# Kernel optimization log

Measured on AMD Instinct MI355X. Metric: run time of the kernel, lower is better.

The kernel has to match this reference:

```python
import jax, jax.numpy as jnp
import numpy as np

D = 1024
H = 16
HD = D // H  # 64


def setup_inputs() -> dict:
    key = jax.random.key(0)
    ks = jax.random.split(key, 12)
    B, S = 2, 2048
    inp = {
        "input_query": jax.random.normal(ks[0], (B, S, D), jnp.float32),
        "input_key": jax.random.normal(ks[1], (B, S, D), jnp.float32),
        "input_value": jax.random.normal(ks[2], (B, S, D), jnp.float32),
        "mask": jnp.ones((S, S), dtype=bool),  # ignored, as in original
        # per-head Q/K/V linears, stacked over heads: [H, D, HD]
        "Wq": jax.random.normal(ks[3], (H, D, HD), jnp.float32) / np.sqrt(D),
        "bq": jax.random.normal(ks[4], (H, HD), jnp.float32) * 0.01,
        "Wk": jax.random.normal(ks[5], (H, D, HD), jnp.float32) / np.sqrt(D),
        "bk": jax.random.normal(ks[6], (H, HD), jnp.float32) * 0.01,
        "Wv": jax.random.normal(ks[7], (H, D, HD), jnp.float32) / np.sqrt(D),
        "bv": jax.random.normal(ks[8], (H, HD), jnp.float32) * 0.01,
        "Wo": jax.random.normal(ks[9], (D, D), jnp.float32) / np.sqrt(D),
        "bo": jax.random.normal(ks[10], (D,), jnp.float32) * 0.01,
    }
    return inp


def reference(input_query, input_key, input_value, mask, Wq, bq, Wk, bk, Wv, bv, Wo, bo):
    B, S, _ = input_query.shape
    # batched per-head projections: [B,S,D] x [H,D,HD] -> [B,H,S,HD]
    q = jnp.einsum("bsd,hdk->bhsk", input_query, Wq) + bq[None, :, None, :]
    k = jnp.einsum("bsd,hdk->bhsk", input_key, Wk) + bk[None, :, None, :]
    v = jnp.einsum("bsd,hdk->bhsk", input_value, Wv) + bv[None, :, None, :]
    scale = 1.0 / np.sqrt(HD)
    scores = jnp.einsum("bhqk,bhsk->bhqs", q, k) * scale  # [B,H,S,S]
    causal = jnp.tril(jnp.ones((S, S), dtype=bool))
    scores = jnp.where(causal[None, None], scores, jnp.finfo(scores.dtype).min)
    p = jax.nn.softmax(scores, axis=-1)
    out = jnp.einsum("bhqs,bhsk->bhqk", p, v)  # [B,H,S,HD]
    # concat heads (matches torch.cat over head outputs on last dim)
    out = out.transpose(0, 2, 1, 3).reshape(B, S, D)
    return out @ Wo + bo
```

## Files before the change

kernel.cpp:

```cpp
#include <hip/hip_runtime.h>
#include <hip/hip_bf16.h>

typedef __bf16 bf16;
typedef bf16 bf16x8 __attribute__((ext_vector_type(8)));
typedef bf16 bf16x4 __attribute__((ext_vector_type(4)));
typedef float f32x4 __attribute__((ext_vector_type(4)));

#define B_  2
#define S_  2048
#define D_  1024
#define H_  16
#define HD_ 64
#define M_  4096
#define K_  1024
#define N_  1024

#if __has_builtin(__builtin_amdgcn_exp2f)
#define EXP2F(x) __builtin_amdgcn_exp2f(x)
#else
#define EXP2F(x) exp2f(x)
#endif

__device__ __forceinline__ void gld16(const bf16* g, bf16* l) {
    __builtin_amdgcn_global_load_lds(
        (const __attribute__((address_space(1))) unsigned int*)(g),
        (__attribute__((address_space(3))) unsigned int*)(l), 16, 0, 0);
}
__device__ __forceinline__ void gld16f(const float* g, float* l) {
    __builtin_amdgcn_global_load_lds(
        (const __attribute__((address_space(1))) unsigned int*)(g),
        (__attribute__((address_space(3))) unsigned int*)(l), 16, 0, 0);
}

__global__ void pack_w(const float* __restrict__ wq, const float* __restrict__ wk,
                       const float* __restrict__ wv, const float* __restrict__ wo,
                       bf16* __restrict__ out) {
    int t = blockIdx.y;
    bf16* dst = out + (size_t)t * N_ * K_;
    int o = blockIdx.x * 256 + threadIdx.x;
    int n = o >> 10, k = o & 1023;
    if (t == 3) {
        dst[o] = (bf16)wo[k * D_ + n];
    } else {
        const float* src = (t == 0) ? wq : (t == 1) ? wk : wv;
        dst[o] = (bf16)src[(n >> 6) * (D_ * HD_) + k * HD_ + (n & 63)];
    }
}

__global__ __launch_bounds__(256) void gemm_qkv(
        const float* __restrict__ xq, const float* __restrict__ xk,
        const float* __restrict__ xv, const bf16* __restrict__ Wt,
        const float* __restrict__ bq, const float* __restrict__ bk,
        const float* __restrict__ bv, bf16* __restrict__ QKV) {
    __shared__ __align__(16) float Af[2][128 * 32];
    __shared__ __align__(16) bf16 Bs[2][128 * 32];
    int t = blockIdx.z;
    const float* A = (t == 0) ? xq : (t == 1) ? xk : xv;
    const bf16* W = Wt + (size_t)t * N_ * K_;
    const float* bias = (t == 0) ? bq : (t == 1) ? bk : bv;
    int m0 = blockIdx.x * 128, n0 = blockIdx.y * 128;
    int tid = threadIdx.x;
    int w = tid >> 6, l = tid & 63, lr = l & 15, lg = l >> 4;
    int wr = (w >> 1) * 64, wc = (w & 1) * 64;
    int srow = (l >> 2), scol = (l & 3) * 8;
    size_t aoff[4];
    #pragma unroll
    for (int c = 0; c < 4; c++) {
        int chunk = w * 256 + c * 64 + l;
        int r = chunk >> 3, p = chunk & 7;
        aoff[c] = (size_t)(m0 + r) * K_ + ((p ^ (r & 7)) << 2);
    }
    f32x4 acc[4][4] = {};
    #pragma unroll
    for (int c = 0; c < 4; c++)
        gld16f(A + aoff[c], &Af[0][(w * 256 + c * 64) * 4]);
    #pragma unroll
    for (int c = 0; c < 2; c++) {
        int chunk = w * 2 + c;
        gld16(&W[(size_t)(n0 + chunk * 16 + srow) * K_ + scol], &Bs[0][chunk * 512]);
    }
    __syncthreads();
    for (int k0 = 0; k0 < K_; k0 += 32) {
        int cur = (k0 >> 5) & 1, nxt = cur ^ 1;
        if (k0 + 32 < K_) {
            #pragma unroll
            for (int c = 0; c < 4; c++)
                gld16f(A + aoff[c] + k0 + 32, &Af[nxt][(w * 256 + c * 64) * 4]);
            #pragma unroll
            for (int c = 0; c < 2; c++) {
                int chunk = w * 2 + c;
                gld16(&W[(size_t)(n0 + chunk * 16 + srow) * K_ + k0 + 32 + scol], &Bs[nxt][chunk * 512]);
            }
        }
        bf16x8 af[4], bfr[4];
        #pragma unroll
        for (int mi = 0; mi < 4; mi++) {
            int r = wr + mi * 16 + lr;
            f32x4 a0 = *(const f32x4*)((const char*)Af[cur] + r * 128 + (((lg * 2) ^ (r & 7)) * 16));
            f32x4 a1 = *(const f32x4*)((const char*)Af[cur] + r * 128 + (((lg * 2 + 1) ^ (r & 7)) * 16));
            bf16x8 v = { (bf16)a0[0], (bf16)a0[1], (bf16)a0[2], (bf16)a0[3],
                         (bf16)a1[0], (bf16)a1[1], (bf16)a1[2], (bf16)a1[3] };
            af[mi] = v;
        }
        #pragma unroll
        for (int ni = 0; ni < 4; ni++) bfr[ni] = *(const bf16x8*)&Bs[cur][(wc + ni * 16 + lr) * 32 + lg * 8];
        #pragma unroll
        for (int mi = 0; mi < 4; mi++)
            #pragma unroll
            for (int ni = 0; ni < 4; ni++)
                acc[mi][ni] = __builtin_amdgcn_mfma_f32_16x16x32_bf16(af[mi], bfr[ni], acc[mi][ni], 0, 0, 0);
        __syncthreads();
    }
    float qscale = (t == 0) ? 0.125f * 1.4426950408889634f : 1.0f;
    #pragma unroll
    for (int mi = 0; mi < 4; mi++)
        #pragma unroll
        for (int ni = 0; ni < 4; ni++)
            #pragma unroll
            for (int i = 0; i < 4; i++) {
                int m = m0 + wr + mi * 16 + lg * 4 + i;
                int n = n0 + wc + ni * 16 + lr;
                float v = (acc[mi][ni][i] + bias[n]) * qscale;
                int b = m >> 11, s = m & 2047, h = n >> 6, hd = n & 63;
                QKV[((((size_t)t * B_ + b) * H_ + h) * S_ + s) * HD_ + hd] = (bf16)v;
            }
}

__global__ __launch_bounds__(256) void gemm_out(
        const bf16* __restrict__ A, const bf16* __restrict__ Wt,
        const float* __restrict__ bo, float* __restrict__ out) {
    __shared__ __align__(16) bf16 As[2][128 * 32];
    __shared__ __align__(16) bf16 Bs[2][128 * 32];
    int m0 = blockIdx.x * 128, n0 = blockIdx.y * 128;
    int tid = threadIdx.x;
    int w = tid >> 6, l = tid & 63, lr = l & 15, lg = l >> 4;
    int wr = (w >> 1) * 64, wc = (w & 1) * 64;
    int srow = (l >> 2), scol = (l & 3) * 8;
    f32x4 acc[4][4] = {};
    #pragma unroll
    for (int c = 0; c < 2; c++) {
        int chunk = w * 2 + c;
        gld16(&A[(size_t)(m0 + chunk * 16 + srow) * K_ + scol], &As[0][chunk * 512]);
        gld16(&Wt[(size_t)(n0 + chunk * 16 + srow) * K_ + scol], &Bs[0][chunk * 512]);
    }
    __syncthreads();
    for (int k0 = 0; k0 < K_; k0 += 32) {
        int cur = (k0 >> 5) & 1, nxt = cur ^ 1;
        if (k0 + 32 < K_) {
            #pragma unroll
            for (int c = 0; c < 2; c++) {
                int chunk = w * 2 + c;
                gld16(&A[(size_t)(m0 + chunk * 16 + srow) * K_ + k0 + 32 + scol], &As[nxt][chunk * 512]);
                gld16(&Wt[(size_t)(n0 + chunk * 16 + srow) * K_ + k0 + 32 + scol], &Bs[nxt][chunk * 512]);
            }
        }
        bf16x8 af[4], bfr[4];
        #pragma unroll
        for (int mi = 0; mi < 4; mi++) af[mi] = *(const bf16x8*)&As[cur][(wr + mi * 16 + lr) * 32 + lg * 8];
        #pragma unroll
        for (int ni = 0; ni < 4; ni++) bfr[ni] = *(const bf16x8*)&Bs[cur][(wc + ni * 16 + lr) * 32 + lg * 8];
        #pragma unroll
        for (int mi = 0; mi < 4; mi++)
            #pragma unroll
            for (int ni = 0; ni < 4; ni++)
                acc[mi][ni] = __builtin_amdgcn_mfma_f32_16x16x32_bf16(af[mi], bfr[ni], acc[mi][ni], 0, 0, 0);
        __syncthreads();
    }
    #pragma unroll
    for (int mi = 0; mi < 4; mi++)
        #pragma unroll
        for (int ni = 0; ni < 4; ni++)
            #pragma unroll
            for (int i = 0; i < 4; i++) {
                int m = m0 + wr + mi * 16 + lg * 4 + i;
                int n = n0 + wc + ni * 16 + lr;
                out[(size_t)m * N_ + n] = acc[mi][ni][i] + bo[n];
            }
}

__global__ __launch_bounds__(256) void transpose_v(const bf16* __restrict__ V,
                                                   bf16* __restrict__ VT) {
    __shared__ __align__(16) bf16 Ls[64][64];
    int s0 = blockIdx.x * 64, bh = blockIdx.y;
    const bf16* src = V + (size_t)bh * S_ * HD_;
    bf16* dst = VT + (size_t)bh * HD_ * S_;
    int tid = threadIdx.x;
    #pragma unroll
    for (int c = tid; c < 512; c += 256) {
        int row = c >> 3, cg = (c & 7) * 8;
        int cgp = cg ^ (((row >> 3) & 3) << 4);
        *(bf16x8*)&Ls[row][cgp] = *(const bf16x8*)&src[(size_t)(s0 + row) * 64 + cg];
    }
    __syncthreads();
    #pragma unroll
    for (int c = tid; c < 512; c += 256) {
        int hd = c >> 3, sg = (c & 7) * 8;
        bf16x8 v;
        #pragma unroll
        for (int e = 0; e < 8; e++) {
            int row = sg + e;
            v[e] = Ls[row][hd ^ (((row >> 3) & 3) << 4)];
        }
        *(bf16x8*)&dst[(size_t)hd * S_ + s0 + sg] = v;
    }
}

__global__ __launch_bounds__(512) void attn(const bf16* __restrict__ QKV,
                                            const bf16* __restrict__ VT,
                                            bf16* __restrict__ AO) {
    __shared__ __align__(16) bf16 Ks[2][64][72];
    __shared__ __align__(16) bf16 Vts[2][64][72];
    __shared__ __align__(16) bf16 Ps[8][16][72];
    int bh = blockIdx.y;
    int qt = (bh & 16) ? blockIdx.x : (15 - blockIdx.x);
    int q0 = qt * 128;
    const bf16* Qp = QKV + (size_t)bh * S_ * HD_;
    const bf16* Kp = QKV + (size_t)(32 + bh) * S_ * HD_;
    const bf16* VTp = VT + (size_t)bh * HD_ * S_;
    int tid = threadIdx.x, w = tid >> 6, l = tid & 63, lr = l & 15, lg = l >> 4;
    int srow = tid >> 3, scg = (tid & 7) * 8;

    bf16x8 aq[2];
    #pragma unroll
    for (int ks = 0; ks < 2; ks++)
        aq[ks] = *(const bf16x8*)&Qp[(size_t)(q0 + w * 16 + lr) * 64 + ks * 32 + lg * 8];

    f32x4 o[4] = {};
    float lsum[4] = {};
    int jmax = 2 * qt + 1;

    *(bf16x8*)&Ks[0][srow][scg]  = *(const bf16x8*)&Kp[(size_t)srow * 64 + scg];
    *(bf16x8*)&Vts[0][srow][scg] = *(const bf16x8*)&VTp[(size_t)srow * S_ + scg];
    __syncthreads();

    for (int j = 0; j <= jmax; ++j) {
        int cur = j & 1;
        bool pf = (j < jmax);
        bf16x8 kreg, vreg;
        if (pf) {
            kreg = *(const bf16x8*)&Kp[(size_t)((j + 1) * 64 + srow) * 64 + scg];
            vreg = *(const bf16x8*)&VTp[(size_t)srow * S_ + (j + 1) * 64 + scg];
        }

        f32x4 sc[4] = {};
        __builtin_amdgcn_s_setprio(1);
        #pragma unroll
        for (int ks = 0; ks < 2; ks++)
            #pragma unroll
            for (int ni = 0; ni < 4; ni++) {
                bf16x8 bk_ = *(const bf16x8*)&Ks[cur][ni * 16 + lr][ks * 32 + lg * 8];
                sc[ni] = __builtin_amdgcn_mfma_f32_16x16x32_bf16(aq[ks], bk_, sc[ni], 0, 0, 0);
            }
        __builtin_amdgcn_s_setprio(0);

        bool diag = (j >= 2 * qt);
        int qrow = w * 16 + lg * 4;
        int kvb = j * 64 - q0;
        #pragma unroll
        for (int ni = 0; ni < 4; ni++)
            #pragma unroll
            for (int i = 0; i < 4; i++) {
                float s = sc[ni][i];
                if (diag && (kvb + ni * 16 + lr > qrow + i)) s = -30000.0f;
                float p = EXP2F(s);
                lsum[i] += p;
                Ps[w][lg * 4 + i][ni * 16 + lr] = (bf16)p;
            }

        __builtin_amdgcn_s_setprio(1);
        #pragma unroll
        for (int ks = 0; ks < 2; ks++) {
            bf16x8 ap = *(const bf16x8*)&Ps[w][lr][ks * 32 + lg * 8];
            #pragma unroll
            for (int nf = 0; nf < 4; nf++) {
                bf16x8 bv_ = *(const bf16x8*)&Vts[cur][nf * 16 + lr][ks * 32 + lg * 8];
                o[nf] = __builtin_amdgcn_mfma_f32_16x16x32_bf16(ap, bv_, o[nf], 0, 0, 0);
            }
        }
        __builtin_amdgcn_s_setprio(0);

        if (pf) {
            *(bf16x8*)&Ks[cur ^ 1][srow][scg]  = kreg;
            *(bf16x8*)&Vts[cur ^ 1][srow][scg] = vreg;
        }
        __syncthreads();
    }

    #pragma unroll
    for (int i = 0; i < 4; i++) {
        #pragma unroll
        for (int xm = 1; xm < 16; xm <<= 1) lsum[i] += __shfl_xor(lsum[i], xm);
    }

    int b = bh >> 4, h = bh & 15;
    #pragma unroll
    for (int i = 0; i < 4; i++) {
        float inv = 1.0f / lsum[i];
        #pragma unroll
        for (int nf = 0; nf < 4; nf++) {
            int m = b * S_ + q0 + w * 16 + lg * 4 + i;
            int d = h * 64 + nf * 16 + lr;
            AO[(size_t)m * D_ + d] = (bf16)(o[nf][i] * inv);
        }
    }
}

extern "C" void kernel_launch(void* const* d_in, const int* in_sizes, int n_in,
                              void* d_out, int out_size, void* d_ws, size_t ws_size,
                              hipStream_t stream) {
    const float* xq = (const float*)d_in[0];
    const float* xk = (const float*)d_in[1];
    const float* xv = (const float*)d_in[2];
    const float* wq = (const float*)d_in[4];
    const float* bq = (const float*)d_in[5];
    const float* wk = (const float*)d_in[6];
    const float* bk = (const float*)d_in[7];
    const float* wv = (const float*)d_in[8];
    const float* bv = (const float*)d_in[9];
    const float* wo = (const float*)d_in[10];
    const float* bo = (const float*)d_in[11];
    float* out = (float*)d_out;

    bf16* Xb  = (bf16*)d_ws;
    bf16* Wb  = Xb  + (size_t)3 * M_ * K_;
    bf16* WoT = Wb  + (size_t)3 * N_ * K_;
    bf16* QKV = WoT + (size_t)N_ * K_;
    bf16* AO  = QKV + (size_t)3 * M_ * K_;
    bf16* VT  = Xb;

    pack_w <<<dim3(N_ * K_ / 256, 4), 256, 0, stream>>>(wq, wk, wv, wo, Wb);
    gemm_qkv<<<dim3(M_ / 128, N_ / 128, 3), 256, 0, stream>>>(xq, xk, xv, Wb, bq, bk, bv, QKV);
    transpose_v<<<dim3(S_ / 64, B_ * H_), 256, 0, stream>>>(QKV + (size_t)2 * M_ * K_, VT);
    attn    <<<dim3(S_ / 128, B_ * H_), 512, 0, stream>>>(QKV, VT, AO);
    gemm_out<<<dim3(M_ / 128, N_ / 128), 256, 0, stream>>>(AO, WoT, bo, out);
}
```

Baseline: 131.5 us.

## Convert QKV activations to bf16 in registers and swizzle LDS tiles

The QKV projection GEMM now loads fp32 activations into registers, converts them to bf16, and writes them to a padded bf16 LDS tile. Before, the fp32 data was staged in LDS through direct global-to-LDS loads and converted on every fragment read. Both GEMMs also apply an XOR swizzle to the weight (and output A) LDS tiles to reduce bank conflicts, and peel the last k-step out of the loop. This halves LDS footprint for A in the QKV kernel, but the register-staged loads may expose global latency that the async LDS path hid.

```diff
diff --git a/kernel.cpp b/kernel.cpp
--- a/kernel.cpp
+++ b/kernel.cpp
@@ -22,11 +22,6 @@
 #endif
 
 __device__ __forceinline__ void gld16(const bf16* g, bf16* l) {
-    __builtin_amdgcn_global_load_lds(
-        (const __attribute__((address_space(1))) unsigned int*)(g),
-        (__attribute__((address_space(3))) unsigned int*)(l), 16, 0, 0);
-}
-__device__ __forceinline__ void gld16f(const float* g, float* l) {
     __builtin_amdgcn_global_load_lds(
         (const __attribute__((address_space(1))) unsigned int*)(g),
         (__attribute__((address_space(3))) unsigned int*)(l), 16, 0, 0);
@@ -52,7 +47,7 @@
         const float* __restrict__ xv, const bf16* __restrict__ Wt,
         const float* __restrict__ bq, const float* __restrict__ bk,
         const float* __restrict__ bv, bf16* __restrict__ QKV) {
-    __shared__ __align__(16) float Af[2][128 * 32];
+    __shared__ __align__(16) bf16 As[2][128 * 40];
     __shared__ __align__(16) bf16 Bs[2][128 * 32];
     int t = blockIdx.z;
     const float* A = (t == 0) ? xq : (t == 1) ? xk : xv;
@@ -62,55 +57,81 @@
     int tid = threadIdx.x;
     int w = tid >> 6, l = tid & 63, lr = l & 15, lg = l >> 4;
     int wr = (w >> 1) * 64, wc = (w & 1) * 64;
-    int srow = (l >> 2), scol = (l & 3) * 8;
-    size_t aoff[4];
-    #pragma unroll
-    for (int c = 0; c < 4; c++) {
-        int chunk = w * 256 + c * 64 + l;
-        int r = chunk >> 3, p = chunk & 7;
-        aoff[c] = (size_t)(m0 + r) * K_ + ((p ^ (r & 7)) << 2);
-    }
+    int ar = tid >> 1, ah = tid & 1;
+    const float* agp = A + (size_t)(m0 + ar) * K_ + ah * 16;
+    int awb = ar * 80 + ah * 32;
+    int srow = l >> 2;
+    int sscol = ((l & 3) ^ ((srow >> 1) & 3)) * 8;
+    int boff[4];
+    #pragma unroll
+    for (int ni = 0; ni < 4; ni++) {
+        int row = wc + ni * 16 + lr;
+        boff[ni] = row * 64 + ((lg ^ ((row >> 1) & 3)) * 16);
+    }
+    int aoffr[4];
+    #pragma unroll
+    for (int mi = 0; mi < 4; mi++) aoffr[mi] = (wr + mi * 16 + lr) * 80 + lg * 16;
+
     f32x4 acc[4][4] = {};
-    #pragma unroll
-    for (int c = 0; c < 4; c++)
-        gld16f(A + aoff[c], &Af[0][(w * 256 + c * 64) * 4]);
-    #pragma unroll
-    for (int c = 0; c < 2; c++) {
-        int chunk = w * 2 + c;
-        gld16(&W[(size_t)(n0 + chunk * 16 + srow) * K_ + scol], &Bs[0][chunk * 512]);
+
+    {
+        float4 av0 = *(const float4*)(agp + 0);
+        float4 av1 = *(const float4*)(agp + 4);
+        float4 av2 = *(const float4*)(agp + 8);
+        float4 av3 = *(const float4*)(agp + 12);
+        #pragma unroll
+        for (int c = 0; c < 2; c++) {
+            int chunk = w * 2 + c;
+            gld16(&W[(size_t)(n0 + chunk * 16 + srow) * K_ + sscol], &Bs[0][chunk * 512]);
+        }
+        bf16x8 b0 = { (bf16)av0.x, (bf16)av0.y, (bf16)av0.z, (bf16)av0.w,
+                      (bf16)av1.x, (bf16)av1.y, (bf16)av1.z, (bf16)av1.w };
+        bf16x8 b1 = { (bf16)av2.x, (bf16)av2.y, (bf16)av2.z, (bf16)av2.w,
+                      (bf16)av3.x, (bf16)av3.y, (bf16)av3.z, (bf16)av3.w };
+        *(bf16x8*)((char*)As[0] + awb)      = b0;
+        *(bf16x8*)((char*)As[0] + awb + 16) = b1;
     }
     __syncthreads();
-    for (int k0 = 0; k0 < K_; k0 += 32) {
-        int cur = (k0 >> 5) & 1, nxt = cur ^ 1;
-        if (k0 + 32 < K_) {
-            #pragma unroll
-            for (int c = 0; c < 4; c++)
-                gld16f(A + aoff[c] + k0 + 32, &Af[nxt][(w * 256 + c * 64) * 4]);
-            #pragma unroll
-            for (int c = 0; c < 2; c++) {
-                int chunk = w * 2 + c;
-                gld16(&W[(size_t)(n0 + chunk * 16 + srow) * K_ + k0 + 32 + scol], &Bs[nxt][chunk * 512]);
-            }
-        }
+
+    auto do_step = [&](int cb, int k0) {
         bf16x8 af[4], bfr[4];
         #pragma unroll
-        for (int mi = 0; mi < 4; mi++) {
-            int r = wr + mi * 16 + lr;
-            f32x4 a0 = *(const f32x4*)((const char*)Af[cur] + r * 128 + (((lg * 2) ^ (r & 7)) * 16));
-            f32x4 a1 = *(const f32x4*)((const char*)Af[cur] + r * 128 + (((lg * 2 + 1) ^ (r & 7)) * 16));
-            bf16x8 v = { (bf16)a0[0], (bf16)a0[1], (bf16)a0[2], (bf16)a0[3],
-                         (bf16)a1[0], (bf16)a1[1], (bf16)a1[2], (bf16)a1[3] };
-            af[mi] = v;
-        }
-        #pragma unroll
-        for (int ni = 0; ni < 4; ni++) bfr[ni] = *(const bf16x8*)&Bs[cur][(wc + ni * 16 + lr) * 32 + lg * 8];
+        for (int mi = 0; mi < 4; mi++)
+            af[mi] = *(const bf16x8*)((const char*)As[cb] + aoffr[mi]);
+        #pragma unroll
+        for (int ni = 0; ni < 4; ni++)
+            bfr[ni] = *(const bf16x8*)((const char*)Bs[cb] + boff[ni]);
         #pragma unroll
         for (int mi = 0; mi < 4; mi++)
             #pragma unroll
             for (int ni = 0; ni < 4; ni++)
                 acc[mi][ni] = __builtin_amdgcn_mfma_f32_16x16x32_bf16(af[mi], bfr[ni], acc[mi][ni], 0, 0, 0);
+    };
+
+    int cur = 0;
+    for (int k0 = 0; k0 < K_ - 32; k0 += 32) {
+        int nxt = cur ^ 1;
+        float4 av0 = *(const float4*)(agp + k0 + 32);
+        float4 av1 = *(const float4*)(agp + k0 + 36);
+        float4 av2 = *(const float4*)(agp + k0 + 40);
+        float4 av3 = *(const float4*)(agp + k0 + 44);
+        #pragma unroll
+        for (int c = 0; c < 2; c++) {
+            int chunk = w * 2 + c;
+            gld16(&W[(size_t)(n0 + chunk * 16 + srow) * K_ + k0 + 32 + sscol], &Bs[nxt][chunk * 512]);
+        }
+        do_step(cur, k0);
+        bf16x8 b0 = { (bf16)av0.x, (bf16)av0.y, (bf16)av0.z, (bf16)av0.w,
+                      (bf16)av1.x, (bf16)av1.y, (bf16)av1.z, (bf16)av1.w };
+        bf16x8 b1 = { (bf16)av2.x, (bf16)av2.y, (bf16)av2.z, (bf16)av2.w,
+                      (bf16)av3.x, (bf16)av3.y, (bf16)av3.z, (bf16)av3.w };
+        *(bf16x8*)((char*)As[nxt] + awb)      = b0;
+        *(bf16x8*)((char*)As[nxt] + awb + 16) = b1;
         __syncthreads();
-    }
+        cur = nxt;
+    }
+    do_step(cur, K_ - 32);
+
     float qscale = (t == 0) ? 0.125f * 1.4426950408889634f : 1.0f;
     #pragma unroll
     for (int mi = 0; mi < 4; mi++)
@@ -135,37 +156,52 @@
     int tid = threadIdx.x;
     int w = tid >> 6, l = tid & 63, lr = l & 15, lg = l >> 4;
     int wr = (w >> 1) * 64, wc = (w & 1) * 64;
-    int srow = (l >> 2), scol = (l & 3) * 8;
+    int srow = l >> 2;
+    int sscol = ((l & 3) ^ ((srow >> 1) & 3)) * 8;
+    int aoff[4], boff[4];
+    #pragma unroll
+    for (int i = 0; i < 4; i++) {
+        int ra = wr + i * 16 + lr, rb = wc + i * 16 + lr;
+        aoff[i] = ra * 64 + ((lg ^ ((ra >> 1) & 3)) * 16);
+        boff[i] = rb * 64 + ((lg ^ ((rb >> 1) & 3)) * 16);
+    }
     f32x4 acc[4][4] = {};
     #pragma unroll
     for (int c = 0; c < 2; c++) {
         int chunk = w * 2 + c;
-        gld16(&A[(size_t)(m0 + chunk * 16 + srow) * K_ + scol], &As[0][chunk * 512]);
-        gld16(&Wt[(size_t)(n0 + chunk * 16 + srow) * K_ + scol], &Bs[0][chunk * 512]);
+        gld16(&A[(size_t)(m0 + chunk * 16 + srow) * K_ + sscol], &As[0][chunk * 512]);
+        gld16(&Wt[(size_t)(n0 + chunk * 16 + srow) * K_ + sscol], &Bs[0][chunk * 512]);
     }
     __syncthreads();
-    for (int k0 = 0; k0 < K_; k0 += 32) {
-        int cur = (k0 >> 5) & 1, nxt = cur ^ 1;
-        if (k0 + 32 < K_) {
-            #pragma unroll
-            for (int c = 0; c < 2; c++) {
-                int chunk = w * 2 + c;
-                gld16(&A[(size_t)(m0 + chunk * 16 + srow) * K_ + k0 + 32 + scol], &As[nxt][chunk * 512]);
-                gld16(&Wt[(size_t)(n0 + chunk * 16 + srow) * K_ + k0 + 32 + scol], &Bs[nxt][chunk * 512]);
-            }
-        }
+
+    auto do_step = [&](int cb) {
         bf16x8 af[4], bfr[4];
         #pragma unroll
-        for (int mi = 0; mi < 4; mi++) af[mi] = *(const bf16x8*)&As[cur][(wr + mi * 16 + lr) * 32 + lg * 8];
-        #pragma unroll
-        for (int ni = 0; ni < 4; ni++) bfr[ni] = *(const bf16x8*)&Bs[cur][(wc + ni * 16 + lr) * 32 + lg * 8];
+        for (int mi = 0; mi < 4; mi++) af[mi] = *(const bf16x8*)((const char*)As[cb] + aoff[mi]);
+        #pragma unroll
+        for (int ni = 0; ni < 4; ni++) bfr[ni] = *(const bf16x8*)((const char*)Bs[cb] + boff[ni]);
         #pragma unroll
         for (int mi = 0; mi < 4; mi++)
             #pragma unroll
             for (int ni = 0; ni < 4; ni++)
                 acc[mi][ni] = __builtin_amdgcn_mfma_f32_16x16x32_bf16(af[mi], bfr[ni], acc[mi][ni], 0, 0, 0);
+    };
+
+    int cur = 0;
+    for (int k0 = 0; k0 < K_ - 32; k0 += 32) {
+        int nxt = cur ^ 1;
+        #pragma unroll
+        for (int c = 0; c < 2; c++) {
+            int chunk = w * 2 + c;
+            gld16(&A[(size_t)(m0 + chunk * 16 + srow) * K_ + k0 + 32 + sscol], &As[nxt][chunk * 512]);
+            gld16(&Wt[(size_t)(n0 + chunk * 16 + srow) * K_ + k0 + 32 + sscol], &Bs[nxt][chunk * 512]);
+        }
+        do_step(cur);
         __syncthreads();
-    }
+        cur = nxt;
+    }
+    do_step(cur);
+
     #pragma unroll
     for (int mi = 0; mi < 4; mi++)
         #pragma unroll
```

Result: slower. 144.2 us (+9.7%).
